# Kernel tuning notes

Hardware: AMD Instinct MI355X
Metric: run time of the kernel (lower is better)

## Reference

```python
import jax, jax.numpy as jnp
import numpy as np

B, P, D = 64, 256, 768
S = P + 1            # class token + patches
GRID = 16.0          # sqrt(no_of_patches)
N_IMGS = 10000


def setup_inputs() -> dict:
    key = jax.random.key(0)
    ks = jax.random.split(key, 10)
    sc = 1.0 / np.sqrt(D)
    return {
        "x": jax.random.normal(ks[0], (B, S, D), jnp.float32),
        "img_ids": jax.random.randint(ks[1], (B,), 0, N_IMGS),
        "mask": jnp.ones((B, S), jnp.int32),
        "avgs": 0.1 * jax.random.normal(ks[2], (N_IMGS, 2, P), jnp.float32),
        "std_devs": jnp.ones((N_IMGS, 2, P), jnp.float32),
        "Wq": sc * jax.random.normal(ks[3], (D, D), jnp.float32),
        "bq": jnp.zeros((D,), jnp.float32),
        "Wk": sc * jax.random.normal(ks[4], (D, D), jnp.float32),
        "bk": jnp.zeros((D,), jnp.float32),
        "Wv": sc * jax.random.normal(ks[5], (D, D), jnp.float32),
        "bv": jnp.zeros((D,), jnp.float32),
        "noise_x": jax.random.normal(ks[6], (B, P), jnp.float32),  # torch.normal(0, sigma)
        "noise_y": jax.random.normal(ks[7], (B, P), jnp.float32),
    }


def reference(x, img_ids, mask, avgs, std_devs, Wq, bq, Wk, bk, Wv, bv, noise_x, noise_y):
    # nn.Linear: y = x @ W^T + b
    q = jnp.einsum("bsd,ed->bse", x, Wq) + bq  # (B,S,D)
    k = jnp.einsum("bsd,ed->bse", x, Wk) + bk
    v = jnp.einsum("bsd,ed->bse", x, Wv) + bv

    a = avgs[img_ids]       # (B,2,P)
    sd = std_devs[img_ids]  # (B,2,P)
    half = (GRID - 1.0) / 2.0
    kx = half * (1.0 + jnp.tanh((noise_x + a[:, 0]) * sd[:, 0]))  # (B,P) in (0, GRID-1)
    ky = half * (1.0 + jnp.tanh((noise_y + a[:, 1]) * sd[:, 1]))
    kx1, kx2 = jnp.ceil(kx), jnp.floor(kx)
    ky1, ky2 = jnp.ceil(ky), jnp.floor(ky)

    # corner order matches original: (x1,y1), (x2,y1), (x1,y2), (x2,y2)
    cx = jnp.stack([kx1, kx2, kx1, kx2], axis=1)  # (B,4,P)
    cy = jnp.stack([ky1, ky1, ky2, ky2], axis=1)
    idxs = jax.lax.stop_gradient(GRID * cy + cx).astype(jnp.int32)  # (B,4,P), < P

    sk = jnp.take_along_axis(k[:, None], idxs[..., None], axis=2)  # (B,4,P,D)
    sv = jnp.take_along_axis(v[:, None], idxs[..., None], axis=2)
    cls = jnp.ones((B, 4, 1, D), sk.dtype)
    skf = jnp.concatenate([cls, sk], axis=2)  # (B,4,S,D)
    svf = jnp.concatenate([cls, sv], axis=2)

    # score per query s against its 4 sampled corner keys; softmax over the 4 corners
    scores = jnp.einsum("bnsd,bsd->bsn", skf, q)   # (B,S,4)
    attn = jax.nn.softmax(scores, axis=-1)          # (B,S,4)
    attn_v = attn.transpose(0, 2, 1)[..., None] * svf  # (B,4,S,D)

    # bilinear weights (1-|cx-kx|)*(1-|cy-ky|); class-token weight fixed to 1
    w = (1.0 - jnp.abs(cx - kx[:, None])) * (1.0 - jnp.abs(cy - ky[:, None]))  # (B,4,P)
    wf = jnp.concatenate([jnp.ones((B, 4, 1), w.dtype), w], axis=2)  # (B,4,S)
    out = jnp.einsum("bns,bnsd->bsd", wf, attn_v)  # (B,S,D)
    return out
```

## Files before the change

### kernel.cpp

```cpp
#include <hip/hip_runtime.h>
#include <math.h>


typedef _Float16 f16x8 __attribute__((ext_vector_type(8)));
typedef _Float16 f16x4 __attribute__((ext_vector_type(4)));
typedef float    f32x4 __attribute__((ext_vector_type(4)));

#define MTOT 16448
#define DD   768
#define NC   2304
#define KT   24
#define XCH (129*24*512)
#define WCH (18*24*512)

__global__ __launch_bounds__(256) void prepass(
    const float* __restrict__ x,
    const float* __restrict__ Wq, const float* __restrict__ Wk, const float* __restrict__ Wv,
    _Float16* __restrict__ xp, _Float16* __restrict__ wp)
{
    const int gidx = blockIdx.x * 256 + threadIdx.x;
    const float* src;
    _Float16* dst;
    if (gidx < XCH) {
        const int c = gidx & 511, kk = (gidx >> 9) % KT, t = gidx / (KT * 512);
        const int row = ((c >> 6) << 4) + (c & 15);
        int gm = t * 128 + row; gm = gm < MTOT ? gm : MTOT - 1;
        src = x + (size_t)gm * DD + kk * 32 + ((c >> 4) & 3) * 8;
        dst = xp + (size_t)gidx * 8;
    } else {
        const int g = gidx - XCH;
        const int c = g & 511, kk = (g >> 9) % KT, t = g / (KT * 512);
        const int wrow = t * 128 + ((c >> 6) << 4) + (c & 15);
        const float* W = wrow < 768 ? Wq : (wrow < 1536 ? Wk : Wv);
        const int srow = wrow - (wrow < 768 ? 0 : (wrow < 1536 ? 768 : 1536));
        src = W + (size_t)srow * DD + kk * 32 + ((c >> 4) & 3) * 8;
        dst = wp + (size_t)g * 8;
    }
    const float4 a = *(const float4*)src;
    const float4 b = *(const float4*)(src + 4);
    f16x8 o;
    o[0] = (_Float16)a.x; o[1] = (_Float16)a.y; o[2] = (_Float16)a.z; o[3] = (_Float16)a.w;
    o[4] = (_Float16)b.x; o[5] = (_Float16)b.y; o[6] = (_Float16)b.z; o[7] = (_Float16)b.w;
    *(f16x8*)dst = o;
}

#define GLD(srcp, ldsp) \
    __builtin_amdgcn_global_load_lds( \
        (const __attribute__((address_space(1))) void*)(srcp), \
        (__attribute__((address_space(3))) void*)(ldsp), 16, 0, 0)

__global__ __launch_bounds__(512, 4) void qkv_gemm(
    const _Float16* __restrict__ xp, const _Float16* __restrict__ wp,
    const float* __restrict__ bq, const float* __restrict__ bk, const float* __restrict__ bv,
    _Float16* __restrict__ qkv)
{
    __shared__ __align__(16) _Float16 Ax[4096];
    __shared__ __align__(16) _Float16 Bx[4096];

    const int bid = blockIdx.x;
    const int xcd = bid & 7, pos = bid >> 3;
    const int q8 = 2322 / 8, r8 = 2322 % 8;
    const int orig = (xcd < r8) ? xcd * (q8 + 1) + pos
                                : r8 * (q8 + 1) + (xcd - r8) * q8 + pos;
    const int tileM = orig / 18, tileN = orig % 18;

    const int tid = threadIdx.x, lane = tid & 63, wid = tid >> 6;
    const int wm = wid >> 2, wn = wid & 3;
    const int r16 = lane & 15, kq = lane >> 4;

    const _Float16* Asrc = xp + (size_t)tileM * KT * 4096;
    const _Float16* Bsrc = wp + (size_t)tileN * KT * 4096;

    const f32x4 zero = {0.f, 0.f, 0.f, 0.f};
    f32x4 acc[4][2];
    #pragma unroll
    for (int i = 0; i < 4; ++i)
        #pragma unroll
        for (int j = 0; j < 2; ++j) acc[i][j] = zero;

    for (int kk = 0; kk < KT; ++kk) {
        __syncthreads();
        {
            const int c0 = wid * 64;
            GLD(Asrc + ((size_t)kk * 512 + c0 + lane) * 8, &Ax[c0 * 8]);
            GLD(Bsrc + ((size_t)kk * 512 + c0 + lane) * 8, &Bx[c0 * 8]);
        }
        __syncthreads();

        f16x8 a[4], b[2];
        #pragma unroll
        for (int i = 0; i < 4; ++i)
            a[i] = *(const f16x8*)(&Ax[((wm * 4 + i) * 64 + lane) * 8]);
        #pragma unroll
        for (int j = 0; j < 2; ++j)
            b[j] = *(const f16x8*)(&Bx[((wn * 2 + j) * 64 + lane) * 8]);
        #pragma unroll
        for (int i = 0; i < 4; ++i)
            #pragma unroll
            for (int j = 0; j < 2; ++j)
                acc[i][j] = __builtin_amdgcn_mfma_f32_16x16x32_f16(a[i], b[j], acc[i][j], 0, 0, 0);
    }

    const int sec = tileN / 6;
    const float* bias = sec == 0 ? bq : (sec == 1 ? bk : bv);
    const int bcol0 = (tileN % 6) * 128 + wn * 32;
    #pragma unroll
    for (int i = 0; i < 4; ++i) {
        const int row0 = tileM * 128 + wm * 64 + i * 16 + kq * 4;
        #pragma unroll
        for (int j = 0; j < 2; ++j) {
            const int col = tileN * 128 + wn * 32 + j * 16 + r16;
            const float bb = bias[bcol0 + j * 16 + r16];
            #pragma unroll
            for (int tt = 0; tt < 4; ++tt) {
                const int row = row0 + tt;
                if (row < MTOT)
                    qkv[(size_t)row * NC + col] = (_Float16)(acc[i][j][tt] + bb);
            }
        }
    }
}

__global__ __launch_bounds__(256) void attn_gather(
    const _Float16* __restrict__ qkv,
    const int*   __restrict__ ids,
    const float* __restrict__ avgs,
    const float* __restrict__ stds,
    const float* __restrict__ nx,
    const float* __restrict__ ny,
    float* __restrict__ out)
{
    const int tid  = threadIdx.x;
    const int lane = tid & 63;
    const int bid = blockIdx.x;
    const int swz = (bid & 7) * 514 + (bid >> 3);
    const int gid = swz * 4 + (tid >> 6);
    const int b = gid / 257, s = gid % 257;
    float* orow = out + (size_t)gid * DD;

    if (s == 0) {
        const float4 one = make_float4(1.f, 1.f, 1.f, 1.f);
        #pragma unroll
        for (int j = 0; j < 3; ++j)
            *(float4*)(orow + 4 * lane + 256 * j) = one;
        return;
    }
    const int p   = s - 1;
    const int img = ids[b];
    const size_t ab = (size_t)img * 512 + p;
    const float a0 = avgs[ab], a1 = avgs[ab + 256];
    const float s0 = stds[ab], s1 = stds[ab + 256];
    const float kx = 7.5f * (1.f + tanhf((nx[b * 256 + p] + a0) * s0));
    const float ky = 7.5f * (1.f + tanhf((ny[b * 256 + p] + a1) * s1));
    const float kx1 = ceilf(kx), kx2 = floorf(kx);
    const float ky1 = ceilf(ky), ky2 = floorf(ky);
    const float cx[4] = {kx1, kx2, kx1, kx2};
    const float cy[4] = {ky1, ky1, ky2, ky2};
    int   idx[4];
    float w[4];
    #pragma unroll
    for (int n = 0; n < 4; ++n) {
        idx[n] = (int)(16.f * cy[n] + cx[n]);
        w[n]   = (1.f - fabsf(cx[n] - kx)) * (1.f - fabsf(cy[n] - ky));
    }

    const _Float16* qrow = qkv + (size_t)gid * NC;
    float qf[12];
    #pragma unroll
    for (int j = 0; j < 3; ++j) {
        const f16x4 v = *(const f16x4*)(qrow + lane * 4 + j * 256);
        qf[4 * j + 0] = (float)v[0]; qf[4 * j + 1] = (float)v[1];
        qf[4 * j + 2] = (float)v[2]; qf[4 * j + 3] = (float)v[3];
    }

    float sc[4];
    #pragma unroll
    for (int n = 0; n < 4; ++n) {
        const _Float16* krow = qkv + (size_t)(b * 257 + idx[n]) * NC + 768;
        float a = 0.f;
        #pragma unroll
        for (int j = 0; j < 3; ++j) {
            const f16x4 kv = *(const f16x4*)(krow + lane * 4 + j * 256);
            a += qf[4 * j + 0] * (float)kv[0] + qf[4 * j + 1] * (float)kv[1]
               + qf[4 * j + 2] * (float)kv[2] + qf[4 * j + 3] * (float)kv[3];
        }
        sc[n] = a;
    }
    #pragma unroll
    for (int n = 0; n < 4; ++n)
        for (int off = 32; off > 0; off >>= 1)
            sc[n] += __shfl_xor(sc[n], off);

    const float mx = fmaxf(fmaxf(sc[0], sc[1]), fmaxf(sc[2], sc[3]));
    const float e0 = expf(sc[0] - mx), e1 = expf(sc[1] - mx),
                e2 = expf(sc[2] - mx), e3 = expf(sc[3] - mx);
    const float inv = 1.f / (e0 + e1 + e2 + e3);
    const float coef[4] = {e0 * inv * w[0], e1 * inv * w[1], e2 * inv * w[2], e3 * inv * w[3]};

    const _Float16* vr0 = qkv + (size_t)(b * 257 + idx[0]) * NC + 1536;
    const _Float16* vr1 = qkv + (size_t)(b * 257 + idx[1]) * NC + 1536;
    const _Float16* vr2 = qkv + (size_t)(b * 257 + idx[2]) * NC + 1536;
    const _Float16* vr3 = qkv + (size_t)(b * 257 + idx[3]) * NC + 1536;
    #pragma unroll
    for (int j = 0; j < 3; ++j) {
        const int d = lane * 4 + j * 256;
        const f16x4 v0 = *(const f16x4*)(vr0 + d);
        const f16x4 v1 = *(const f16x4*)(vr1 + d);
        const f16x4 v2 = *(const f16x4*)(vr2 + d);
        const f16x4 v3 = *(const f16x4*)(vr3 + d);
        float4 o;
        o.x = coef[0] * (float)v0[0] + coef[1] * (float)v1[0] + coef[2] * (float)v2[0] + coef[3] * (float)v3[0];
        o.y = coef[0] * (float)v0[1] + coef[1] * (float)v1[1] + coef[2] * (float)v2[1] + coef[3] * (float)v3[1];
        o.z = coef[0] * (float)v0[2] + coef[1] * (float)v1[2] + coef[2] * (float)v2[2] + coef[3] * (float)v3[2];
        o.w = coef[0] * (float)v0[3] + coef[1] * (float)v1[3] + coef[2] * (float)v2[3] + coef[3] * (float)v3[3];
        *(float4*)(orow + d) = o;
    }
}

extern "C" void kernel_launch(void* const* d_in, const int* in_sizes, int n_in,
                              void* d_out, int out_size, void* d_ws, size_t ws_size,
                              hipStream_t stream) {
    const float* x    = (const float*)d_in[0];
    const int*   ids  = (const int*)  d_in[1];
    const float* avgs = (const float*)d_in[3];
    const float* stds = (const float*)d_in[4];
    const float* Wq   = (const float*)d_in[5];
    const float* bq   = (const float*)d_in[6];
    const float* Wk   = (const float*)d_in[7];
    const float* bk   = (const float*)d_in[8];
    const float* Wv   = (const float*)d_in[9];
    const float* bv   = (const float*)d_in[10];
    const float* nx   = (const float*)d_in[11];
    const float* ny   = (const float*)d_in[12];
    float* out = (float*)d_out;

    char* ws = (char*)d_ws;
    _Float16* qkv = (_Float16*)ws;
    _Float16* xp  = (_Float16*)(ws + 75792384);
    _Float16* wp  = (_Float16*)(ws + 75792384 + 25362432);

    prepass<<<(XCH + WCH) / 256, 256, 0, stream>>>(x, Wq, Wk, Wv, xp, wp);
    qkv_gemm<<<2322, 512, 0, stream>>>(xp, wp, bq, bk, bv, qkv);
    attn_gather<<<4112, 256, 0, stream>>>(qkv, ids, avgs, stds, nx, ny, out);
}
```

Baseline: 120.4 us.

## Triple-buffer LDS tiles in QKV GEMM with prefetch two steps ahead

Replaces the single-buffered LDS staging in the QKV GEMM main loop with a three-stage ring buffer. Global-to-LDS loads are issued two K-steps ahead, with explicit vmcnt waits and a single barrier per iteration instead of two. MFMA issue is also raised in wave priority. The aim is to hide global load latency behind matrix math, at the cost of three times the LDS per block, which may lower occupancy.

```diff
diff --git a/kernel.cpp b/kernel.cpp
--- a/kernel.cpp
+++ b/kernel.cpp
@@ -54,8 +54,8 @@
     const float* __restrict__ bq, const float* __restrict__ bk, const float* __restrict__ bv,
     _Float16* __restrict__ qkv)
 {
-    __shared__ __align__(16) _Float16 Ax[4096];
-    __shared__ __align__(16) _Float16 Bx[4096];
+    __shared__ __align__(16) _Float16 Ax[3][4096];
+    __shared__ __align__(16) _Float16 Bx[3][4096];
 
     const int bid = blockIdx.x;
     const int xcd = bid & 7, pos = bid >> 3;
@@ -70,6 +70,7 @@
 
     const _Float16* Asrc = xp + (size_t)tileM * KT * 4096;
     const _Float16* Bsrc = wp + (size_t)tileN * KT * 4096;
+    const int c0 = wid * 64;
 
     const f32x4 zero = {0.f, 0.f, 0.f, 0.f};
     f32x4 acc[4][2];
@@ -78,27 +79,52 @@
         #pragma unroll
         for (int j = 0; j < 2; ++j) acc[i][j] = zero;
 
-    for (int kk = 0; kk < KT; ++kk) {
-        __syncthreads();
-        {
-            const int c0 = wid * 64;
-            GLD(Asrc + ((size_t)kk * 512 + c0 + lane) * 8, &Ax[c0 * 8]);
-            GLD(Bsrc + ((size_t)kk * 512 + c0 + lane) * 8, &Bx[c0 * 8]);
-        }
-        __syncthreads();
+    #pragma unroll
+    for (int tt = 0; tt < 2; ++tt) {
+        GLD(Asrc + ((size_t)tt * 512 + c0 + lane) * 8, &Ax[tt][c0 * 8]);
+        GLD(Bsrc + ((size_t)tt * 512 + c0 + lane) * 8, &Bx[tt][c0 * 8]);
+    }
+    asm volatile("s_waitcnt vmcnt(2)" ::: "memory");
+    __builtin_amdgcn_sched_barrier(0);
+    __builtin_amdgcn_s_barrier();
+    __builtin_amdgcn_sched_barrier(0);
+
+    for (int t = 0; t < KT; ++t) {
+        const int cur = t % 3;
+        if (t + 2 < KT) {
+            const int nb = (t + 2) % 3;
+            GLD(Asrc + ((size_t)(t + 2) * 512 + c0 + lane) * 8, &Ax[nb][c0 * 8]);
+            GLD(Bsrc + ((size_t)(t + 2) * 512 + c0 + lane) * 8, &Bx[nb][c0 * 8]);
+        }
+        __builtin_amdgcn_sched_barrier(0);
 
         f16x8 a[4], b[2];
         #pragma unroll
         for (int i = 0; i < 4; ++i)
-            a[i] = *(const f16x8*)(&Ax[((wm * 4 + i) * 64 + lane) * 8]);
+            a[i] = *(const f16x8*)(&Ax[cur][((wm * 4 + i) * 64 + lane) * 8]);
         #pragma unroll
         for (int j = 0; j < 2; ++j)
-            b[j] = *(const f16x8*)(&Bx[((wn * 2 + j) * 64 + lane) * 8]);
+            b[j] = *(const f16x8*)(&Bx[cur][((wn * 2 + j) * 64 + lane) * 8]);
+
+        __builtin_amdgcn_s_setprio(1);
         #pragma unroll
         for (int i = 0; i < 4; ++i)
             #pragma unroll
             for (int j = 0; j < 2; ++j)
                 acc[i][j] = __builtin_amdgcn_mfma_f32_16x16x32_f16(a[i], b[j], acc[i][j], 0, 0, 0);
+        __builtin_amdgcn_s_setprio(0);
+        __builtin_amdgcn_sched_barrier(0);
+
+        if (t + 2 < KT) {
+            asm volatile("s_waitcnt vmcnt(2)" ::: "memory");
+        } else if (t + 1 < KT) {
+            asm volatile("s_waitcnt vmcnt(0)" ::: "memory");
+        }
+        if (t + 1 < KT) {
+            __builtin_amdgcn_sched_barrier(0);
+            __builtin_amdgcn_s_barrier();
+            __builtin_amdgcn_sched_barrier(0);
+        }
     }
 
     const int sec = tileN / 6;
```

New measurement: 114.7 us, median of 2. 4.8% less time.

## Software-pipeline QKV GEMM with 4-stage LDS ring and direct B register loads

Applied to the files above, without the earlier changes.

Replaces the single-buffered load/sync/compute loop with a prefetch pipeline. A tiles stream into a 4-deep LDS ring two steps ahead, and B fragments are loaded straight from global memory into double-buffered registers one step ahead. Explicit vmcnt waits, sched barriers and setprio replace the two __syncthreads per k-step, so memory latency can hide behind MFMA work. The cost is more LDS per block, which may lower occupancy, plus fragile hand-counted waitcnts and an unrolled schedule fixed to KT=24.

```diff
diff --git a/kernel.cpp b/kernel.cpp
--- a/kernel.cpp
+++ b/kernel.cpp
@@ -49,13 +49,39 @@
         (const __attribute__((address_space(1))) void*)(srcp), \
         (__attribute__((address_space(3))) void*)(ldsp), 16, 0, 0)
 
+#define SB __builtin_amdgcn_sched_barrier(0)
+
+#define TILE(T, BUF, BU, BL, B2, STA, STB, VMN, BAR) do {                            \
+    if (STB) {                                                                       \
+        bS[BL][0] = *(const f16x8*)(Bsrc + ((size_t)(T + 1) * 512 + wn * 128 + lane) * 8);      \
+        bS[BL][1] = *(const f16x8*)(Bsrc + ((size_t)(T + 1) * 512 + wn * 128 + 64 + lane) * 8); \
+    }                                                                                \
+    SB;                                                                              \
+    if (STA) GLD(Asrc + ((size_t)(T + 2) * 512 + c0 + lane) * 8, &Ax[B2][c0 * 8]);   \
+    SB;                                                                              \
+    {                                                                                \
+        f16x8 a_[4];                                                                 \
+        _Pragma("unroll") for (int i_ = 0; i_ < 4; ++i_)                             \
+            a_[i_] = *(const f16x8*)(&Ax[BUF][((wm * 4 + i_) * 64 + lane) * 8]);     \
+        __builtin_amdgcn_s_setprio(1);                                               \
+        _Pragma("unroll") for (int i_ = 0; i_ < 4; ++i_) {                           \
+            acc[i_][0] = __builtin_amdgcn_mfma_f32_16x16x32_f16(a_[i_], bS[BU][0], acc[i_][0], 0, 0, 0); \
+            acc[i_][1] = __builtin_amdgcn_mfma_f32_16x16x32_f16(a_[i_], bS[BU][1], acc[i_][1], 0, 0, 0); \
+        }                                                                            \
+        __builtin_amdgcn_s_setprio(0);                                               \
+    }                                                                                \
+    SB;                                                                              \
+    if ((VMN) == 3) asm volatile("s_waitcnt vmcnt(3)" ::: "memory");                 \
+    else if ((VMN) == 2) asm volatile("s_waitcnt vmcnt(2)" ::: "memory");            \
+    if (BAR) { SB; __builtin_amdgcn_s_barrier(); SB; }                               \
+} while (0)
+
 __global__ __launch_bounds__(512, 4) void qkv_gemm(
     const _Float16* __restrict__ xp, const _Float16* __restrict__ wp,
     const float* __restrict__ bq, const float* __restrict__ bk, const float* __restrict__ bv,
     _Float16* __restrict__ qkv)
 {
-    __shared__ __align__(16) _Float16 Ax[4096];
-    __shared__ __align__(16) _Float16 Bx[4096];
+    __shared__ __align__(16) _Float16 Ax[4][4096];
 
     const int bid = blockIdx.x;
     const int xcd = bid & 7, pos = bid >> 3;
@@ -70,6 +96,7 @@
 
     const _Float16* Asrc = xp + (size_t)tileM * KT * 4096;
     const _Float16* Bsrc = wp + (size_t)tileN * KT * 4096;
+    const int c0 = wid * 64;
 
     const f32x4 zero = {0.f, 0.f, 0.f, 0.f};
     f32x4 acc[4][2];
@@ -78,28 +105,33 @@
         #pragma unroll
         for (int j = 0; j < 2; ++j) acc[i][j] = zero;
 
-    for (int kk = 0; kk < KT; ++kk) {
-        __syncthreads();
-        {
-            const int c0 = wid * 64;
-            GLD(Asrc + ((size_t)kk * 512 + c0 + lane) * 8, &Ax[c0 * 8]);
-            GLD(Bsrc + ((size_t)kk * 512 + c0 + lane) * 8, &Bx[c0 * 8]);
-        }
-        __syncthreads();
-
-        f16x8 a[4], b[2];
-        #pragma unroll
-        for (int i = 0; i < 4; ++i)
-            a[i] = *(const f16x8*)(&Ax[((wm * 4 + i) * 64 + lane) * 8]);
-        #pragma unroll
-        for (int j = 0; j < 2; ++j)
-            b[j] = *(const f16x8*)(&Bx[((wn * 2 + j) * 64 + lane) * 8]);
-        #pragma unroll
-        for (int i = 0; i < 4; ++i)
-            #pragma unroll
-            for (int j = 0; j < 2; ++j)
-                acc[i][j] = __builtin_amdgcn_mfma_f32_16x16x32_f16(a[i], b[j], acc[i][j], 0, 0, 0);
-    }
+    f16x8 bS[2][2];
+
+    GLD(Asrc + (size_t)(c0 + lane) * 8, &Ax[0][c0 * 8]);
+    GLD(Asrc + ((size_t)512 + c0 + lane) * 8, &Ax[1][c0 * 8]);
+    SB;
+    bS[0][0] = *(const f16x8*)(Bsrc + (size_t)(wn * 128 + lane) * 8);
+    bS[0][1] = *(const f16x8*)(Bsrc + (size_t)(wn * 128 + 64 + lane) * 8);
+    SB;
+    asm volatile("s_waitcnt vmcnt(3)" ::: "memory");
+    SB;
+    __builtin_amdgcn_s_barrier();
+    SB;
+
+    TILE(0, 0, 0, 1, 2, 1, 1, 3, 1);
+
+    #pragma unroll 1
+    for (int it = 0; it < 5; ++it) {
+        const int t0 = 4 * it + 1;
+        TILE(t0 + 0, 1, 1, 0, 3, 1, 1, 3, 1);
+        TILE(t0 + 1, 2, 0, 1, 0, 1, 1, 3, 1);
+        TILE(t0 + 2, 3, 1, 0, 1, 1, 1, 3, 1);
+        TILE(t0 + 3, 0, 0, 1, 2, 1, 1, 3, 1);
+    }
+
+    TILE(21, 1, 1, 0, 3, 1, 1, 3, 1);
+    TILE(22, 2, 0, 1, 0, 0, 1, 2, 1);
+    TILE(23, 3, 1, 0, 0, 0, 0, -1, 0);
 
     const int sec = tileN / 6;
     const float* bias = sec == 0 ? bq : (sec == 1 ? bk : bv);
```

Result: no change. 122.8 us (+1.9%).
